# Optimization experiments

Measured on AMD Instinct MI355X. Metric: run time of the kernel, lower is better.

The kernel has to match this reference:

```python
import jax, jax.numpy as jnp
import numpy as np
import math

TAU = 0.5        # module stores self.tau = 1.0 / tau with tau=2.0
THRESHOLD = 1.0
SURR_C = 1.0 / (2.0 * math.sqrt(2.0 * math.pi))  # coefficient in Stochastic.backward


@jax.custom_vjp
def spike(v):
    # Stochastic.forward: (input > 0).float()
    return (v > 0).astype(v.dtype)


def _spike_fwd(v):
    return spike(v), v


def _spike_bwd(v, g):
    # Stochastic.backward: grad * 1/(2*sqrt(2*pi)) * exp(-v^2/2)
    return (g * (SURR_C * jnp.exp(-0.5 * v * v)),)


spike.defvjp(_spike_fwd, _spike_bwd)


def setup_inputs() -> dict:
    key = jax.random.key(0)
    x = jax.random.normal(key, (32, 128, 8192), dtype=jnp.float32)  # [B, T, N]
    return {"x": x}


def reference(x):
    # Eval-mode iterative stochastic-LIF update (no noise injection).
    xt = jnp.swapaxes(x, 0, 1)  # [T, B, N] for scan over time

    def step(u, x_t):
        u = TAU * u + x_t                # leaky integrate
        o = spike(u - THRESHOLD)         # fire
        u = u * (1.0 - o)                # hard reset by multiply
        return u, o

    u0 = jnp.zeros_like(xt[0])
    _, o = jax.lax.scan(step, u0, xt)
    return jnp.swapaxes(o, 0, 1)  # [B, T, N]
```

## Files before the change

kernel.cpp:

```cpp
#include <hip/hip_runtime.h>
#include <stdint.h>


constexpr int B    = 32;
constexpr int T    = 128;
constexpr int N    = 8192;
constexpr int N4   = N / 4;
constexpr int TC   = 16;
constexpr int NC   = T / TC;
constexpr int NW4  = 64;
constexpr int RING = 4;

__device__ __forceinline__ void async16(void* lds_dst, const void* g_src) {
    __builtin_amdgcn_global_load_lds(
        (const __attribute__((address_space(1))) void*)g_src,
        (__attribute__((address_space(3))) void*)lds_dst, 16, 0, 0);
}

__device__ __forceinline__ void wait_barrier(int vm) {
    if (vm == 8)      asm volatile("s_waitcnt vmcnt(8)\n\ts_barrier" ::: "memory");
    else if (vm == 4) asm volatile("s_waitcnt vmcnt(4)\n\ts_barrier" ::: "memory");
    else              asm volatile("s_waitcnt vmcnt(0)\n\ts_barrier" ::: "memory");
}

__global__ __launch_bounds__(256) void lif_kernel(const float4* __restrict__ x,
                                                  float* __restrict__ out) {
    __shared__ float4 buf[RING][TC][NW4];

    const int tid   = threadIdx.x;
    const int wave  = tid >> 6;
    const int lane  = tid & 63;
    const int b     = blockIdx.x >> 5;
    const int ntile = blockIdx.x & 31;
    const size_t xbase4 = (size_t)b * T * N4 + (size_t)ntile * NW4;
    const size_t obase  = (size_t)b * T * N  + (size_t)ntile * (NW4 * 4) + tid;
    const float4* gx = x + xbase4;

    #pragma unroll
    for (int c = 0; c < 3; ++c) {
        #pragma unroll
        for (int k = 0; k < 4; ++k) {
            const int t_sub = k * 4 + wave;
            async16(&buf[c][t_sub][lane], gx + (size_t)(c * TC + t_sub) * N4 + lane);
        }
    }

    float u = 0.f;
    uint32_t sw[4] = {0u, 0u, 0u, 0u};

    #pragma unroll
    for (int c = 0; c < NC; ++c) {
        const int last = (c + 2 < NC - 1) ? (c + 2) : (NC - 1);
        wait_barrier(4 * (last - c));

        if (c + 3 < NC) {
            #pragma unroll
            for (int k = 0; k < 4; ++k) {
                const int t_sub = k * 4 + wave;
                async16(&buf[(c + 3) & (RING - 1)][t_sub][lane],
                        gx + (size_t)((c + 3) * TC + t_sub) * N4 + lane);
            }
        }

        const float* lb = (const float*)buf[c & (RING - 1)];
        #pragma unroll
        for (int t = 0; t < TC; ++t) {
            const float xt = lb[t * 256 + tid];
            u = 0.5f * u + xt;
            const uint32_t bit = (u > 1.0f) ? 1u : 0u;
            sw[c >> 1] |= bit << ((c & 1) * 16 + t);
            u = (u > 1.0f) ? 0.0f : u;
        }
    }

    #pragma unroll
    for (int t = 0; t < T; ++t) {
        const float sp = ((sw[t >> 5] >> (t & 31)) & 1u) ? 1.0f : 0.0f;
        out[obase + (size_t)t * N] = sp;
    }
}

extern "C" void kernel_launch(void* const* d_in, const int* in_sizes, int n_in,
                              void* d_out, int out_size, void* d_ws, size_t ws_size,
                              hipStream_t stream) {
    const float4* x  = (const float4*)d_in[0];
    float*      out = (float*)d_out;
    const int nblocks = B * (N / (NW4 * 4));
    lif_kernel<<<nblocks, 256, 0, stream>>>(x, out);
}
```

Before: 230.3 us.

## Replace LDS ring with per-thread float4 register pipeline and nontemporal vector stores

Each thread now owns four adjacent neurons and keeps a 16-deep register pipeline of float4 loads across time steps, replacing the LDS async-load ring and its barriers. Spikes are written immediately as float4 nontemporal stores instead of being bit-packed and emitted as scalar stores at the end. Block size drops to 128 threads with half as many blocks, which reduces occupancy but raises per-thread memory parallelism and widens store transactions.

```diff
diff --git a/kernel.cpp b/kernel.cpp
--- a/kernel.cpp
+++ b/kernel.cpp
@@ -2,81 +2,74 @@
 #include <stdint.h>
 
 
-constexpr int B    = 32;
-constexpr int T    = 128;
-constexpr int N    = 8192;
-constexpr int N4   = N / 4;
-constexpr int TC   = 16;
-constexpr int NC   = T / TC;
-constexpr int NW4  = 64;
-constexpr int RING = 4;
+constexpr int B  = 32;
+constexpr int T  = 128;
+constexpr int N  = 8192;
+constexpr int N4 = N / 4;
+constexpr int THREADS = 128;
+constexpr int SPAN4   = THREADS;
+constexpr int NTILES  = N4 / SPAN4;
+constexpr int DP      = 16;
+constexpr int NG      = T / DP;
 
-__device__ __forceinline__ void async16(void* lds_dst, const void* g_src) {
-    __builtin_amdgcn_global_load_lds(
-        (const __attribute__((address_space(1))) void*)g_src,
-        (__attribute__((address_space(3))) void*)lds_dst, 16, 0, 0);
+typedef float v4f __attribute__((ext_vector_type(4)));
+
+__device__ __forceinline__ float lif1(float& u, float x) {
+    u = 0.5f * u + x;
+    const bool s = u > 1.0f;
+    const float o = s ? 1.0f : 0.0f;
+    u = s ? 0.0f : u;
+    return o;
 }
 
-__device__ __forceinline__ void wait_barrier(int vm) {
-    if (vm == 8)      asm volatile("s_waitcnt vmcnt(8)\n\ts_barrier" ::: "memory");
-    else if (vm == 4) asm volatile("s_waitcnt vmcnt(4)\n\ts_barrier" ::: "memory");
-    else              asm volatile("s_waitcnt vmcnt(0)\n\ts_barrier" ::: "memory");
+__device__ __forceinline__ void nt_store4(const float4& o, float4* p) {
+    __builtin_nontemporal_store(*(const v4f*)&o, (v4f*)p);
 }
 
-__global__ __launch_bounds__(256) void lif_kernel(const float4* __restrict__ x,
-                                                  float* __restrict__ out) {
-    __shared__ float4 buf[RING][TC][NW4];
+__global__ __launch_bounds__(THREADS) void lif_kernel(const float4* __restrict__ x,
+                                                      float4* __restrict__ out) {
+    const int tid   = threadIdx.x;
+    const int b     = blockIdx.x >> 4;
+    const int ntile = blockIdx.x & (NTILES - 1);
+    const uint32_t base4 = (uint32_t)b * (T * N4) + (uint32_t)ntile * SPAN4 + tid;
+    const float4* gx = x + base4;
+    float4*       go = out + base4;
 
-    const int tid   = threadIdx.x;
-    const int wave  = tid >> 6;
-    const int lane  = tid & 63;
-    const int b     = blockIdx.x >> 5;
-    const int ntile = blockIdx.x & 31;
-    const size_t xbase4 = (size_t)b * T * N4 + (size_t)ntile * NW4;
-    const size_t obase  = (size_t)b * T * N  + (size_t)ntile * (NW4 * 4) + tid;
-    const float4* gx = x + xbase4;
+    float4 pipe[DP];
+    #pragma unroll
+    for (int k = 0; k < DP; ++k) pipe[k] = gx[(uint32_t)k * N4];
 
-    #pragma unroll
-    for (int c = 0; c < 3; ++c) {
+    float ux = 0.f, uy = 0.f, uz = 0.f, uw = 0.f;
+
+    #pragma unroll 1
+    for (int g = 0; g < NG - 1; ++g) {
+        const uint32_t roff = (uint32_t)(g + 1) * (DP * N4);
+        const uint32_t woff = (uint32_t)g * (DP * N4);
         #pragma unroll
-        for (int k = 0; k < 4; ++k) {
-            const int t_sub = k * 4 + wave;
-            async16(&buf[c][t_sub][lane], gx + (size_t)(c * TC + t_sub) * N4 + lane);
+        for (int k = 0; k < DP; ++k) {
+            const float4 v = pipe[k];
+            pipe[k] = gx[roff + (uint32_t)k * N4];
+            float4 o;
+            o.x = lif1(ux, v.x);
+            o.y = lif1(uy, v.y);
+            o.z = lif1(uz, v.z);
+            o.w = lif1(uw, v.w);
+            nt_store4(o, go + woff + (uint32_t)k * N4);
         }
     }
 
-    float u = 0.f;
-    uint32_t sw[4] = {0u, 0u, 0u, 0u};
-
-    #pragma unroll
-    for (int c = 0; c < NC; ++c) {
-        const int last = (c + 2 < NC - 1) ? (c + 2) : (NC - 1);
-        wait_barrier(4 * (last - c));
-
-        if (c + 3 < NC) {
-            #pragma unroll
-            for (int k = 0; k < 4; ++k) {
-                const int t_sub = k * 4 + wave;
-                async16(&buf[(c + 3) & (RING - 1)][t_sub][lane],
-                        gx + (size_t)((c + 3) * TC + t_sub) * N4 + lane);
-            }
+    {
+        const uint32_t woff = (uint32_t)(NG - 1) * (DP * N4);
+        #pragma unroll
+        for (int k = 0; k < DP; ++k) {
+            const float4 v = pipe[k];
+            float4 o;
+            o.x = lif1(ux, v.x);
+            o.y = lif1(uy, v.y);
+            o.z = lif1(uz, v.z);
+            o.w = lif1(uw, v.w);
+            nt_store4(o, go + woff + (uint32_t)k * N4);
         }
-
-        const float* lb = (const float*)buf[c & (RING - 1)];
-        #pragma unroll
-        for (int t = 0; t < TC; ++t) {
-            const float xt = lb[t * 256 + tid];
-            u = 0.5f * u + xt;
-            const uint32_t bit = (u > 1.0f) ? 1u : 0u;
-            sw[c >> 1] |= bit << ((c & 1) * 16 + t);
-            u = (u > 1.0f) ? 0.0f : u;
-        }
-    }
-
-    #pragma unroll
-    for (int t = 0; t < T; ++t) {
-        const float sp = ((sw[t >> 5] >> (t & 31)) & 1u) ? 1.0f : 0.0f;
-        out[obase + (size_t)t * N] = sp;
     }
 }
 
@@ -84,7 +77,6 @@
                               void* d_out, int out_size, void* d_ws, size_t ws_size,
                               hipStream_t stream) {
     const float4* x  = (const float4*)d_in[0];
-    float*      out = (float*)d_out;
-    const int nblocks = B * (N / (NW4 * 4));
-    lif_kernel<<<nblocks, 256, 0, stream>>>(x, out);
+    float4*      out = (float4*)d_out;
+    lif_kernel<<<B * NTILES, THREADS, 0, stream>>>(x, out);
 }
```

Measured after the change: 241.3 us. 1.05x slower.
